# Kernel tuning notes

Hardware: AMD Instinct MI355X
Metric: run time of the kernel (lower is better)

The kernel has to match this reference:

```python
import jax, jax.numpy as jnp
import numpy as np

N_NODES = 100000
N_EDGES = 3200000
N_FEAT = 256
N_CLASS = 4


def setup_inputs() -> dict:
    key = jax.random.key(0)
    ks = jax.random.split(key, 8)
    x = jax.random.normal(ks[0], (N_NODES, N_FEAT), dtype=jnp.float32)
    edge_index = jax.random.randint(ks[1], (2, N_EDGES), 0, N_NODES, dtype=jnp.int64)
    def xavier(k, shape):
        fan_in, fan_out = shape
        std = np.sqrt(2.0 / (fan_in + fan_out))
        return jax.random.normal(k, shape, dtype=jnp.float32) * std
    return {
        'x': x,
        'edge_index': edge_index,
        'W_gcn': xavier(ks[2], (N_FEAT, 64)),
        'b_gcn': jnp.zeros((64,), jnp.float32),
        'W1': xavier(ks[3], (64, 32)),
        'b1': jnp.zeros((32,), jnp.float32),
        'W2': xavier(ks[4], (32, 16)),
        'b2': jnp.zeros((16,), jnp.float32),
        'W3': xavier(ks[5], (16, N_CLASS)),
        'b3': jnp.zeros((N_CLASS,), jnp.float32),
    }


def gcn_conv(x, edge_index, W, b):
    # PyG GCNConv: transform, add self-loops, symmetric normalization, scatter-add
    N = x.shape[0]
    h = x @ W  # [N, 64]
    loop = jnp.arange(N, dtype=edge_index.dtype)
    src = jnp.concatenate([edge_index[0], loop])
    dst = jnp.concatenate([edge_index[1], loop])
    deg = jax.ops.segment_sum(jnp.ones_like(dst, dtype=h.dtype), dst, num_segments=N)
    dinv = jnp.where(deg > 0, jax.lax.rsqrt(deg), 0.0)
    norm = dinv[src] * dinv[dst]  # [E+N]
    msgs = h[src] * norm[:, None]  # gather [E+N, 64]
    out = jax.ops.segment_sum(msgs, dst, num_segments=N)
    return out + b


def reference(x, edge_index, W_gcn, b_gcn, W1, b1, W2, b2, W3, b3):
    h = gcn_conv(x, edge_index, W_gcn, b_gcn)
    h = jax.nn.relu(h)          # dropout is identity in eval mode
    h = jax.nn.relu(h @ W1 + b1)
    h = jax.nn.relu(h @ W2 + b2)
    h = h @ W3 + b3
    return jax.nn.log_softmax(h, axis=1)
```

## Files before the change

### kernel.cpp

```cpp
#include <hip/hip_runtime.h>
#include <hip/hip_bf16.h>

#define NN 100000
#define NE 3200000
#define NPB 64
#define NB 1564
#define CAP 2560
#define BATCH 8192
#define NGB 1563

typedef __hip_bfloat16 bf16;
typedef __attribute__((ext_vector_type(8))) short bf16x8;
typedef __attribute__((ext_vector_type(4))) float f32x4;

__device__ __forceinline__ void fma4(float4& a, float s, const float4 w) {
  a.x = fmaf(s, w.x, a.x);
  a.y = fmaf(s, w.y, a.y);
  a.z = fmaf(s, w.z, a.z);
  a.w = fmaf(s, w.w, a.w);
}

__device__ __forceinline__ unsigned short f2b(float f) {
  unsigned u = __float_as_uint(f);
  unsigned r = ((u >> 16) & 1u) + 0x7FFFu;
  return (unsigned short)((u + r) >> 16);
}

__device__ __forceinline__ unsigned pack2(float lo, float hi) {
  return (unsigned)f2b(lo) | ((unsigned)f2b(hi) << 16);
}

__global__ __launch_bounds__(1024) void bin_k(const void* __restrict__ eidx,
                                              int* __restrict__ bcur,
                                              int* __restrict__ buckets) {
  __shared__ int scnt[NB];
  __shared__ int sofs[NB];
  __shared__ int sbase[NB];
  __shared__ int lcur[NB];
  __shared__ int tot;
  __shared__ int sflag;
  __shared__ int sorted[BATCH];
  __shared__ int gaddr[BATCH];
  int t = threadIdx.x;
  long long e0 = (long long)blockIdx.x * BATCH;
  int m = (int)((NE - e0 < BATCH) ? (NE - e0) : BATCH);

  if (t < 64) {
    unsigned long long bb = __ballot(((const int*)eidx)[2 * t + 1] == 0);
    if (t == 0) sflag = (bb == 0xFFFFFFFFFFFFFFFFULL) ? 1 : 0;
  }
  for (int i = t; i < NB; i += 1024) scnt[i] = 0;
  if (t == 0) tot = 0;
  __syncthreads();
  int isI64 = sflag;

  int ent[BATCH / 1024], bv[BATCH / 1024];
#pragma unroll
  for (int j = 0; j < BATCH / 1024; j++) {
    int idx = t + j * 1024;
    bv[j] = -1;
    if (idx < m) {
      long long i = e0 + idx;
      int s, d;
      if (isI64) {
        s = (int)((const long long*)eidx)[i];
        d = (int)((const long long*)eidx)[NE + i];
      } else {
        s = ((const int*)eidx)[i];
        d = ((const int*)eidx)[NE + i];
      }
      bv[j] = d >> 6;
      ent[j] = s | ((d & 63) << 17);
      atomicAdd(&scnt[bv[j]], 1);
    }
  }
  __syncthreads();
  for (int i = t; i < NB; i += 1024) {
    int c = scnt[i];
    if (c) {
      sofs[i] = atomicAdd(&tot, c);
      sbase[i] = atomicAdd(&bcur[i], c);
      lcur[i] = sofs[i];
    }
  }
  __syncthreads();
#pragma unroll
  for (int j = 0; j < BATCH / 1024; j++) {
    if (bv[j] >= 0) {
      int pos = atomicAdd(&lcur[bv[j]], 1);
      sorted[pos] = ent[j];
      int gp = sbase[bv[j]] + (pos - sofs[bv[j]]);
      gaddr[pos] = (gp < CAP) ? bv[j] * CAP + gp : -1;
    }
  }
  __syncthreads();
  for (int i = t; i < m; i += 1024) {
    int ga = gaddr[i];
    if (ga >= 0) buckets[ga] = sorted[i];
  }
}

__global__ __launch_bounds__(256) void cnt_k(const int* __restrict__ buckets,
                                             const int* __restrict__ bcur,
                                             float* __restrict__ dinv,
                                             const float* __restrict__ W,
                                             unsigned short* __restrict__ wh,
                                             unsigned short* __restrict__ wl) {
  int b = blockIdx.x, t = threadIdx.x;
  if (b == NB) {
#pragma unroll 4
    for (int i = 0; i < 64; i++) {
      int idx = i * 256 + t;
      int j = idx & 7;
      int lane = (idx >> 3) & 63;
      int pair = idx >> 9;
      int nf = pair & 3, kk = pair >> 2;
      int k = kk * 32 + (lane >> 4) * 8 + j;
      int n = nf * 16 + (lane & 15);
      float w = W[k * 64 + n];
      unsigned short hh = f2b(w);
      float fh = __uint_as_float((unsigned)hh << 16);
      wh[idx] = hh;
      wl[idx] = f2b(w - fh);
    }
    return;
  }
  __shared__ int c4[4][NPB];
  int w = t >> 6;
  if (t < 128) { c4[0][t & 63] = 0; c4[1][t & 63] = 0; }
  else         { c4[2][t & 63] = 0; c4[3][t & 63] = 0; }
  __syncthreads();
  int m = bcur[b]; if (m > CAP) m = CAP;
  const int* bp = buckets + (size_t)b * CAP;
  for (int i = t; i < m; i += 256) atomicAdd(&c4[w][(bp[i] >> 17) & 63], 1);
  __syncthreads();
  int node = b * NPB + t;
  if (t < NPB && node < NN) {
    int s = c4[0][t] + c4[1][t] + c4[2][t] + c4[3][t];
    dinv[node] = rsqrtf((float)s + 1.0f);
  }
}

__global__ __launch_bounds__(256) void gemm_k(const float* __restrict__ x,
                                              const unsigned short* __restrict__ wh,
                                              const unsigned short* __restrict__ wl,
                                              const float* __restrict__ dinv,
                                              bf16* __restrict__ h) {
  int t = threadIdx.x;
  int wv = t >> 6, l = t & 63;
  int rowbase = blockIdx.x * 64 + wv * 16;
  int arow = rowbase + (l & 15);
  if (arow >= NN) arow = NN - 1;
  const float* xrow = x + (size_t)arow * 256 + (l >> 4) * 8;

  const bf16x8* whf = (const bf16x8*)wh;
  const bf16x8* wlf = (const bf16x8*)wl;

  f32x4 acc0 = {0.f, 0.f, 0.f, 0.f};
  f32x4 acc1 = acc0, acc2 = acc0, acc3 = acc0;

  float4 x0a = *(const float4*)(xrow +   0), x0b = *(const float4*)(xrow +   4);
  float4 x1a = *(const float4*)(xrow +  32), x1b = *(const float4*)(xrow +  36);
  float4 x2a = *(const float4*)(xrow +  64), x2b = *(const float4*)(xrow +  68);
  float4 x3a = *(const float4*)(xrow +  96), x3b = *(const float4*)(xrow + 100);
  float4 x4a = *(const float4*)(xrow + 128), x4b = *(const float4*)(xrow + 132);
  float4 x5a = *(const float4*)(xrow + 160), x5b = *(const float4*)(xrow + 164);
  float4 x6a = *(const float4*)(xrow + 192), x6b = *(const float4*)(xrow + 196);
  float4 x7a = *(const float4*)(xrow + 224), x7b = *(const float4*)(xrow + 228);

  bf16x8 ha0, ha1, ha2, ha3, la0, la1, la2, la3;
  bf16x8 hb0, hb1, hb2, hb3, lb0, lb1, lb2, lb3;

#define LOADW(H0, H1, H2, H3, L0, L1, L2, L3, kk)                      \
  {                                                                    \
    int fb_ = (kk) * 256 + l;                                          \
    H0 = whf[fb_]; H1 = whf[fb_ + 64]; H2 = whf[fb_ + 128]; H3 = whf[fb_ + 192]; \
    L0 = wlf[fb_]; L1 = wlf[fb_ + 64]; L2 = wlf[fb_ + 128]; L3 = wlf[fb_ + 192]; \
  }
#define COMPUTE(Xa, Xb, H0, H1, H2, H3, L0, L1, L2, L3)                \
  {                                                                    \
    bf16x8 ah, al;                                                     \
    {                                                                  \
      unsigned short hh_; float fh_;                                   \
      hh_ = f2b(Xa.x); fh_ = __uint_as_float((unsigned)hh_ << 16); ah[0] = (short)hh_; al[0] = (short)f2b(Xa.x - fh_); \
      hh_ = f2b(Xa.y); fh_ = __uint_as_float((unsigned)hh_ << 16); ah[1] = (short)hh_; al[1] = (short)f2b(Xa.y - fh_); \
      hh_ = f2b(Xa.z); fh_ = __uint_as_float((unsigned)hh_ << 16); ah[2] = (short)hh_; al[2] = (short)f2b(Xa.z - fh_); \
      hh_ = f2b(Xa.w); fh_ = __uint_as_float((unsigned)hh_ << 16); ah[3] = (short)hh_; al[3] = (short)f2b(Xa.w - fh_); \
      hh_ = f2b(Xb.x); fh_ = __uint_as_float((unsigned)hh_ << 16); ah[4] = (short)hh_; al[4] = (short)f2b(Xb.x - fh_); \
      hh_ = f2b(Xb.y); fh_ = __uint_as_float((unsigned)hh_ << 16); ah[5] = (short)hh_; al[5] = (short)f2b(Xb.y - fh_); \
      hh_ = f2b(Xb.z); fh_ = __uint_as_float((unsigned)hh_ << 16); ah[6] = (short)hh_; al[6] = (short)f2b(Xb.z - fh_); \
      hh_ = f2b(Xb.w); fh_ = __uint_as_float((unsigned)hh_ << 16); ah[7] = (short)hh_; al[7] = (short)f2b(Xb.w - fh_); \
    }                                                                  \
    acc0 = __builtin_amdgcn_mfma_f32_16x16x32_bf16(ah, H0, acc0, 0, 0, 0); \
    acc1 = __builtin_amdgcn_mfma_f32_16x16x32_bf16(ah, H1, acc1, 0, 0, 0); \
    acc2 = __builtin_amdgcn_mfma_f32_16x16x32_bf16(ah, H2, acc2, 0, 0, 0); \
    acc3 = __builtin_amdgcn_mfma_f32_16x16x32_bf16(ah, H3, acc3, 0, 0, 0); \
    acc0 = __builtin_amdgcn_mfma_f32_16x16x32_bf16(ah, L0, acc0, 0, 0, 0); \
    acc1 = __builtin_amdgcn_mfma_f32_16x16x32_bf16(ah, L1, acc1, 0, 0, 0); \
    acc2 = __builtin_amdgcn_mfma_f32_16x16x32_bf16(ah, L2, acc2, 0, 0, 0); \
    acc3 = __builtin_amdgcn_mfma_f32_16x16x32_bf16(ah, L3, acc3, 0, 0, 0); \
    acc0 = __builtin_amdgcn_mfma_f32_16x16x32_bf16(al, H0, acc0, 0, 0, 0); \
    acc1 = __builtin_amdgcn_mfma_f32_16x16x32_bf16(al, H1, acc1, 0, 0, 0); \
    acc2 = __builtin_amdgcn_mfma_f32_16x16x32_bf16(al, H2, acc2, 0, 0, 0); \
    acc3 = __builtin_amdgcn_mfma_f32_16x16x32_bf16(al, H3, acc3, 0, 0, 0); \
  }
#define SBAR __builtin_amdgcn_sched_barrier(0);

  LOADW(ha0, ha1, ha2, ha3, la0, la1, la2, la3, 0)
  LOADW(hb0, hb1, hb2, hb3, lb0, lb1, lb2, lb3, 1)
  COMPUTE(x0a, x0b, ha0, ha1, ha2, ha3, la0, la1, la2, la3) SBAR
  LOADW(ha0, ha1, ha2, ha3, la0, la1, la2, la3, 2)
  COMPUTE(x1a, x1b, hb0, hb1, hb2, hb3, lb0, lb1, lb2, lb3) SBAR
  LOADW(hb0, hb1, hb2, hb3, lb0, lb1, lb2, lb3, 3)
  COMPUTE(x2a, x2b, ha0, ha1, ha2, ha3, la0, la1, la2, la3) SBAR
  LOADW(ha0, ha1, ha2, ha3, la0, la1, la2, la3, 4)
  COMPUTE(x3a, x3b, hb0, hb1, hb2, hb3, lb0, lb1, lb2, lb3) SBAR
  LOADW(hb0, hb1, hb2, hb3, lb0, lb1, lb2, lb3, 5)
  COMPUTE(x4a, x4b, ha0, ha1, ha2, ha3, la0, la1, la2, la3) SBAR
  LOADW(ha0, ha1, ha2, ha3, la0, la1, la2, la3, 6)
  COMPUTE(x5a, x5b, hb0, hb1, hb2, hb3, lb0, lb1, lb2, lb3) SBAR
  LOADW(hb0, hb1, hb2, hb3, lb0, lb1, lb2, lb3, 7)
  COMPUTE(x6a, x6b, ha0, ha1, ha2, ha3, la0, la1, la2, la3) SBAR
  COMPUTE(x7a, x7b, hb0, hb1, hb2, hb3, lb0, lb1, lb2, lb3)
#undef LOADW
#undef COMPUTE
#undef SBAR

#pragma unroll
  for (int reg = 0; reg < 4; reg++) {
    int row = rowbase + (l >> 4) * 4 + reg;
    if (row < NN) {
      float dn = dinv[row];
      unsigned short* hp = (unsigned short*)h + (size_t)row * 64 + (l & 15);
      hp[0]  = f2b(acc0[reg] * dn);
      hp[16] = f2b(acc1[reg] * dn);
      hp[32] = f2b(acc2[reg] * dn);
      hp[48] = f2b(acc3[reg] * dn);
    }
  }
}

__global__ __launch_bounds__(512) void agg_k(const bf16* __restrict__ h,
                                             const int* __restrict__ buckets,
                                             const int* __restrict__ bcur,
                                             const float* __restrict__ dinv,
                                             const float* __restrict__ bg,
                                             bf16* __restrict__ hg) {
  __shared__ int ents[CAP];
  __shared__ int srt[CAP];
  __shared__ int cnt8[8][NPB];
  __shared__ int wcur[8][NPB];
  __shared__ int cnt[NPB];
  __shared__ int off[NPB];
  int b = blockIdx.x, t = threadIdx.x;
  int w = t >> 6;
  int m = bcur[b]; if (m > CAP) m = CAP;
  const int* bp = buckets + (size_t)b * CAP;
  for (int i = t; i < 8 * NPB; i += 512) ((int*)cnt8)[i] = 0;
  __syncthreads();
  for (int i = t; i < m; i += 512) {
    int e = bp[i];
    ents[i] = e;
    atomicAdd(&cnt8[w][(e >> 17) & 63], 1);
  }
  __syncthreads();
  if (t < NPB) {
    int s = 0;
#pragma unroll
    for (int ww = 0; ww < 8; ww++) { int c = cnt8[ww][t]; wcur[ww][t] = s; s += c; }
    cnt[t] = s;
  }
  __syncthreads();
  if (t == 0) {
    int s = 0;
#pragma unroll
    for (int i = 0; i < NPB; i++) { off[i] = s; s += cnt[i]; }
  }
  __syncthreads();
  if (t < NPB) {
#pragma unroll
    for (int ww = 0; ww < 8; ww++) wcur[ww][t] += off[t];
  }
  __syncthreads();
  for (int i = t; i < m; i += 512) {
    int e = ents[i];
    int pos = atomicAdd(&wcur[w][(e >> 17) & 63], 1);
    srt[pos] = e & 0x1FFFF;
  }
  __syncthreads();

  int g = t >> 3, fl = t & 7;
  int node = b * NPB + g;
  if (node >= NN) return;
  int start = off[g];
  int deg = cnt[g];
  float dn = dinv[node];
  const unsigned short* hu = (const unsigned short*)h;

  float a0 = 0.f, a1 = 0.f, a2 = 0.f, a3 = 0.f,
        a4 = 0.f, a5 = 0.f, a6 = 0.f, a7 = 0.f;

#define ACCV(V)                                                          \
  {                                                                      \
    a0 += __uint_as_float(V.x << 16); a1 += __uint_as_float(V.x & 0xFFFF0000u); \
    a2 += __uint_as_float(V.y << 16); a3 += __uint_as_float(V.y & 0xFFFF0000u); \
    a4 += __uint_as_float(V.z << 16); a5 += __uint_as_float(V.z & 0xFFFF0000u); \
    a6 += __uint_as_float(V.w << 16); a7 += __uint_as_float(V.w & 0xFFFF0000u); \
  }

  int i = 0;
  for (; i + 4 <= deg; i += 4) {
    int s0 = srt[start + i], s1 = srt[start + i + 1];
    int s2 = srt[start + i + 2], s3 = srt[start + i + 3];
    uint4 v0 = *(const uint4*)(hu + (size_t)s0 * 64 + fl * 8);
    uint4 v1 = *(const uint4*)(hu + (size_t)s1 * 64 + fl * 8);
    uint4 v2 = *(const uint4*)(hu + (size_t)s2 * 64 + fl * 8);
    uint4 v3 = *(const uint4*)(hu + (size_t)s3 * 64 + fl * 8);
    ACCV(v0) ACCV(v1) ACCV(v2) ACCV(v3)
  }
  for (; i < deg; i++) {
    int s0 = srt[start + i];
    uint4 v0 = *(const uint4*)(hu + (size_t)s0 * 64 + fl * 8);
    ACCV(v0)
  }
#undef ACCV

  uint4 sv = *(const uint4*)(hu + (size_t)node * 64 + fl * 8);
  const float* bb = bg + fl * 8;
  a0 += __uint_as_float(sv.x << 16); a1 += __uint_as_float(sv.x & 0xFFFF0000u);
  a2 += __uint_as_float(sv.y << 16); a3 += __uint_as_float(sv.y & 0xFFFF0000u);
  a4 += __uint_as_float(sv.z << 16); a5 += __uint_as_float(sv.z & 0xFFFF0000u);
  a6 += __uint_as_float(sv.w << 16); a7 += __uint_as_float(sv.w & 0xFFFF0000u);
  uint4 o;
  o.x = pack2(fmaxf(fmaf(a0, dn, bb[0]), 0.f), fmaxf(fmaf(a1, dn, bb[1]), 0.f));
  o.y = pack2(fmaxf(fmaf(a2, dn, bb[2]), 0.f), fmaxf(fmaf(a3, dn, bb[3]), 0.f));
  o.z = pack2(fmaxf(fmaf(a4, dn, bb[4]), 0.f), fmaxf(fmaf(a5, dn, bb[5]), 0.f));
  o.w = pack2(fmaxf(fmaf(a6, dn, bb[6]), 0.f), fmaxf(fmaf(a7, dn, bb[7]), 0.f));
  *(uint4*)((unsigned short*)hg + (size_t)node * 64 + fl * 8) = o;
}

__global__ __launch_bounds__(256) void mlp_k(const bf16* __restrict__ hg,
                                             const float* __restrict__ W1, const float* __restrict__ b1,
                                             const float* __restrict__ W2, const float* __restrict__ b2,
                                             const float* __restrict__ W3, const float* __restrict__ b3,
                                             float* __restrict__ out) {
  __shared__ float4 sW1[512];
  __shared__ float4 sW2[128];
  __shared__ float4 sW3[16];
  __shared__ float sb1[32], sb2[16], sb3[4];
  int t = threadIdx.x;
  for (int i = t; i < 512; i += 256) sW1[i] = ((const float4*)W1)[i];
  if (t < 128) sW2[t] = ((const float4*)W2)[t];
  if (t < 16)  sW3[t] = ((const float4*)W3)[t];
  if (t < 32)  sb1[t] = b1[t];
  if (t < 16)  sb2[t] = b2[t];
  if (t < 4)   sb3[t] = b3[t];
  __syncthreads();
  int n = blockIdx.x * 256 + t;
  if (n >= NN) return;
  float xr[64];
  const uint4* hp = (const uint4*)(hg + (size_t)n * 64);
#pragma unroll
  for (int i = 0; i < 8; i++) {
    uint4 v = hp[i];
    unsigned uu[4] = {v.x, v.y, v.z, v.w};
#pragma unroll
    for (int j = 0; j < 4; j++) {
      xr[8 * i + 2 * j]     = __uint_as_float(uu[j] << 16);
      xr[8 * i + 2 * j + 1] = __uint_as_float(uu[j] & 0xFFFF0000u);
    }
  }
  float4 a1[8];
#pragma unroll
  for (int j = 0; j < 8; j++) a1[j] = make_float4(sb1[4 * j], sb1[4 * j + 1], sb1[4 * j + 2], sb1[4 * j + 3]);
#pragma unroll
  for (int f = 0; f < 64; f++) {
    float xv = xr[f];
#pragma unroll
    for (int j = 0; j < 8; j++) fma4(a1[j], xv, sW1[f * 8 + j]);
  }
  float r2[32];
#pragma unroll
  for (int j = 0; j < 8; j++) {
    r2[4 * j + 0] = fmaxf(a1[j].x, 0.f);
    r2[4 * j + 1] = fmaxf(a1[j].y, 0.f);
    r2[4 * j + 2] = fmaxf(a1[j].z, 0.f);
    r2[4 * j + 3] = fmaxf(a1[j].w, 0.f);
  }
  float4 a2[4];
#pragma unroll
  for (int j = 0; j < 4; j++) a2[j] = make_float4(sb2[4 * j], sb2[4 * j + 1], sb2[4 * j + 2], sb2[4 * j + 3]);
#pragma unroll
  for (int f = 0; f < 32; f++) {
    float xv = r2[f];
#pragma unroll
    for (int j = 0; j < 4; j++) fma4(a2[j], xv, sW2[f * 4 + j]);
  }
  float r3[16];
#pragma unroll
  for (int j = 0; j < 4; j++) {
    r3[4 * j + 0] = fmaxf(a2[j].x, 0.f);
    r3[4 * j + 1] = fmaxf(a2[j].y, 0.f);
    r3[4 * j + 2] = fmaxf(a2[j].z, 0.f);
    r3[4 * j + 3] = fmaxf(a2[j].w, 0.f);
  }
  float4 a3 = make_float4(sb3[0], sb3[1], sb3[2], sb3[3]);
#pragma unroll
  for (int f = 0; f < 16; f++) fma4(a3, r3[f], sW3[f]);
  float m = fmaxf(fmaxf(a3.x, a3.y), fmaxf(a3.z, a3.w));
  float s = expf(a3.x - m) + expf(a3.y - m) + expf(a3.z - m) + expf(a3.w - m);
  float l = m + logf(s);
  ((float4*)out)[n] = make_float4(a3.x - l, a3.y - l, a3.z - l, a3.w - l);
}

extern "C" void kernel_launch(void* const* d_in, const int* in_sizes, int n_in,
                              void* d_out, int out_size, void* d_ws, size_t ws_size,
                              hipStream_t stream) {
  const float* x  = (const float*)d_in[0];
  const void* eidx = d_in[1];
  const float* Wg = (const float*)d_in[2];
  const float* bg = (const float*)d_in[3];
  const float* W1 = (const float*)d_in[4];
  const float* b1 = (const float*)d_in[5];
  const float* W2 = (const float*)d_in[6];
  const float* b2 = (const float*)d_in[7];
  const float* W3 = (const float*)d_in[8];
  const float* b3 = (const float*)d_in[9];

  char* ws = (char*)d_ws;
  bf16*  h       = (bf16*) (ws + 0);
  bf16*  hg      = (bf16*) (ws + 12800000);
  int*   buckets = (int*)  (ws + 25600000);
  float* dinv    = (float*)(ws + 41615360);
  int*   bcur    = (int*)  (ws + 42415360);
  unsigned short* wh = (unsigned short*)(ws + 12800000);
  unsigned short* wl = (unsigned short*)(ws + 12800000 + 32768);

  hipMemsetAsync(bcur, 0, NB * sizeof(int), stream);
  bin_k<<<(NE + BATCH - 1) / BATCH, 1024, 0, stream>>>(eidx, bcur, buckets);
  cnt_k<<<NB + 1, 256, 0, stream>>>(buckets, bcur, dinv, Wg, wh, wl);
  gemm_k<<<NGB, 256, 0, stream>>>(x, wh, wl, dinv, h);
  agg_k<<<NB, 512, 0, stream>>>(h, buckets, bcur, dinv, bg, hg);
  mlp_k<<<(NN + 255) / 256, 256, 0, stream>>>(hg, W1, b1, W2, b2, W3, b3, (float*)d_out);
}
```

Baseline: 152.3 us.

## Fuse MLP head into aggregation kernel and halve edge binning batch

The MLP and log-softmax head now run inside the aggregation kernel. Each block stages its 64 aggregated rows in fp32 shared memory and lets one wavefront run the three small dense layers per node. This removes the bf16 round trip of hg through global memory and one kernel launch. In exchange only 64 of 512 threads do the MLP work, LDS use grows (about 26 KB more), and occupancy may drop. The binning batch size is also halved, giving bin_k more blocks.

```diff
diff --git a/kernel.cpp b/kernel.cpp
--- a/kernel.cpp
+++ b/kernel.cpp
@@ -6,7 +6,7 @@
 #define NPB 64
 #define NB 1564
 #define CAP 2560
-#define BATCH 8192
+#define BATCH 4096
 #define NGB 1563
 
 typedef __hip_bfloat16 bf16;
@@ -245,17 +245,31 @@
                                              const int* __restrict__ bcur,
                                              const float* __restrict__ dinv,
                                              const float* __restrict__ bg,
-                                             bf16* __restrict__ hg) {
+                                             const float* __restrict__ W1, const float* __restrict__ b1,
+                                             const float* __restrict__ W2, const float* __restrict__ b2,
+                                             const float* __restrict__ W3, const float* __restrict__ b3,
+                                             float* __restrict__ out) {
   __shared__ int ents[CAP];
   __shared__ int srt[CAP];
   __shared__ int cnt8[8][NPB];
   __shared__ int wcur[8][NPB];
   __shared__ int cnt[NPB];
   __shared__ int off[NPB];
+  __shared__ float hrowf[NPB][65];
+  __shared__ float4 sW1f[512];
+  __shared__ float4 sW2f[128];
+  __shared__ float4 sW3f[16];
+  __shared__ float sb1[32], sb2[16], sb3[4];
   int b = blockIdx.x, t = threadIdx.x;
   int w = t >> 6;
   int m = bcur[b]; if (m > CAP) m = CAP;
   const int* bp = buckets + (size_t)b * CAP;
+  if (t < 512) sW1f[t] = ((const float4*)W1)[t];
+  if (t < 128) sW2f[t] = ((const float4*)W2)[t];
+  if (t < 16)  sW3f[t] = ((const float4*)W3)[t];
+  if (t < 32)  sb1[t] = b1[t];
+  if (t < 16)  sb2[t] = b2[t];
+  if (t < 4)   sb3[t] = b3[t];
   for (int i = t; i < 8 * NPB; i += 512) ((int*)cnt8)[i] = 0;
   __syncthreads();
   for (int i = t; i < m; i += 512) {
@@ -291,10 +305,9 @@
 
   int g = t >> 3, fl = t & 7;
   int node = b * NPB + g;
-  if (node >= NN) return;
-  int start = off[g];
-  int deg = cnt[g];
-  float dn = dinv[node];
+  bool valid = node < NN;
+  int start = valid ? off[g] : 0;
+  int deg = valid ? cnt[g] : 0;
   const unsigned short* hu = (const unsigned short*)h;
 
   float a0 = 0.f, a1 = 0.f, a2 = 0.f, a3 = 0.f,
@@ -325,92 +338,74 @@
   }
 #undef ACCV
 
-  uint4 sv = *(const uint4*)(hu + (size_t)node * 64 + fl * 8);
-  const float* bb = bg + fl * 8;
-  a0 += __uint_as_float(sv.x << 16); a1 += __uint_as_float(sv.x & 0xFFFF0000u);
-  a2 += __uint_as_float(sv.y << 16); a3 += __uint_as_float(sv.y & 0xFFFF0000u);
-  a4 += __uint_as_float(sv.z << 16); a5 += __uint_as_float(sv.z & 0xFFFF0000u);
-  a6 += __uint_as_float(sv.w << 16); a7 += __uint_as_float(sv.w & 0xFFFF0000u);
-  uint4 o;
-  o.x = pack2(fmaxf(fmaf(a0, dn, bb[0]), 0.f), fmaxf(fmaf(a1, dn, bb[1]), 0.f));
-  o.y = pack2(fmaxf(fmaf(a2, dn, bb[2]), 0.f), fmaxf(fmaf(a3, dn, bb[3]), 0.f));
-  o.z = pack2(fmaxf(fmaf(a4, dn, bb[4]), 0.f), fmaxf(fmaf(a5, dn, bb[5]), 0.f));
-  o.w = pack2(fmaxf(fmaf(a6, dn, bb[6]), 0.f), fmaxf(fmaf(a7, dn, bb[7]), 0.f));
-  *(uint4*)((unsigned short*)hg + (size_t)node * 64 + fl * 8) = o;
-}
-
-__global__ __launch_bounds__(256) void mlp_k(const bf16* __restrict__ hg,
-                                             const float* __restrict__ W1, const float* __restrict__ b1,
-                                             const float* __restrict__ W2, const float* __restrict__ b2,
-                                             const float* __restrict__ W3, const float* __restrict__ b3,
-                                             float* __restrict__ out) {
-  __shared__ float4 sW1[512];
-  __shared__ float4 sW2[128];
-  __shared__ float4 sW3[16];
-  __shared__ float sb1[32], sb2[16], sb3[4];
-  int t = threadIdx.x;
-  for (int i = t; i < 512; i += 256) sW1[i] = ((const float4*)W1)[i];
-  if (t < 128) sW2[t] = ((const float4*)W2)[t];
-  if (t < 16)  sW3[t] = ((const float4*)W3)[t];
-  if (t < 32)  sb1[t] = b1[t];
-  if (t < 16)  sb2[t] = b2[t];
-  if (t < 4)   sb3[t] = b3[t];
-  __syncthreads();
-  int n = blockIdx.x * 256 + t;
-  if (n >= NN) return;
-  float xr[64];
-  const uint4* hp = (const uint4*)(hg + (size_t)n * 64);
-#pragma unroll
-  for (int i = 0; i < 8; i++) {
-    uint4 v = hp[i];
-    unsigned uu[4] = {v.x, v.y, v.z, v.w};
-#pragma unroll
-    for (int j = 0; j < 4; j++) {
-      xr[8 * i + 2 * j]     = __uint_as_float(uu[j] << 16);
-      xr[8 * i + 2 * j + 1] = __uint_as_float(uu[j] & 0xFFFF0000u);
-    }
-  }
-  float4 a1[8];
-#pragma unroll
-  for (int j = 0; j < 8; j++) a1[j] = make_float4(sb1[4 * j], sb1[4 * j + 1], sb1[4 * j + 2], sb1[4 * j + 3]);
-#pragma unroll
-  for (int f = 0; f < 64; f++) {
-    float xv = xr[f];
-#pragma unroll
-    for (int j = 0; j < 8; j++) fma4(a1[j], xv, sW1[f * 8 + j]);
-  }
-  float r2[32];
-#pragma unroll
-  for (int j = 0; j < 8; j++) {
-    r2[4 * j + 0] = fmaxf(a1[j].x, 0.f);
-    r2[4 * j + 1] = fmaxf(a1[j].y, 0.f);
-    r2[4 * j + 2] = fmaxf(a1[j].z, 0.f);
-    r2[4 * j + 3] = fmaxf(a1[j].w, 0.f);
-  }
-  float4 a2[4];
-#pragma unroll
-  for (int j = 0; j < 4; j++) a2[j] = make_float4(sb2[4 * j], sb2[4 * j + 1], sb2[4 * j + 2], sb2[4 * j + 3]);
-#pragma unroll
-  for (int f = 0; f < 32; f++) {
-    float xv = r2[f];
-#pragma unroll
-    for (int j = 0; j < 4; j++) fma4(a2[j], xv, sW2[f * 4 + j]);
-  }
-  float r3[16];
-#pragma unroll
-  for (int j = 0; j < 4; j++) {
-    r3[4 * j + 0] = fmaxf(a2[j].x, 0.f);
-    r3[4 * j + 1] = fmaxf(a2[j].y, 0.f);
-    r3[4 * j + 2] = fmaxf(a2[j].z, 0.f);
-    r3[4 * j + 3] = fmaxf(a2[j].w, 0.f);
-  }
-  float4 a3 = make_float4(sb3[0], sb3[1], sb3[2], sb3[3]);
-#pragma unroll
-  for (int f = 0; f < 16; f++) fma4(a3, r3[f], sW3[f]);
-  float m = fmaxf(fmaxf(a3.x, a3.y), fmaxf(a3.z, a3.w));
-  float s = expf(a3.x - m) + expf(a3.y - m) + expf(a3.z - m) + expf(a3.w - m);
-  float l = m + logf(s);
-  ((float4*)out)[n] = make_float4(a3.x - l, a3.y - l, a3.z - l, a3.w - l);
+  if (valid) {
+    float dn = dinv[node];
+    uint4 sv = *(const uint4*)(hu + (size_t)node * 64 + fl * 8);
+    const float* bb = bg + fl * 8;
+    a0 += __uint_as_float(sv.x << 16); a1 += __uint_as_float(sv.x & 0xFFFF0000u);
+    a2 += __uint_as_float(sv.y << 16); a3 += __uint_as_float(sv.y & 0xFFFF0000u);
+    a4 += __uint_as_float(sv.z << 16); a5 += __uint_as_float(sv.z & 0xFFFF0000u);
+    a6 += __uint_as_float(sv.w << 16); a7 += __uint_as_float(sv.w & 0xFFFF0000u);
+    float* hr = &hrowf[g][fl * 8];
+    hr[0] = fmaxf(fmaf(a0, dn, bb[0]), 0.f);
+    hr[1] = fmaxf(fmaf(a1, dn, bb[1]), 0.f);
+    hr[2] = fmaxf(fmaf(a2, dn, bb[2]), 0.f);
+    hr[3] = fmaxf(fmaf(a3, dn, bb[3]), 0.f);
+    hr[4] = fmaxf(fmaf(a4, dn, bb[4]), 0.f);
+    hr[5] = fmaxf(fmaf(a5, dn, bb[5]), 0.f);
+    hr[6] = fmaxf(fmaf(a6, dn, bb[6]), 0.f);
+    hr[7] = fmaxf(fmaf(a7, dn, bb[7]), 0.f);
+  }
+  __syncthreads();
+
+  if (t < 64) {
+    int nodem = b * NPB + t;
+    if (nodem < NN) {
+      float4 m1[8];
+#pragma unroll
+      for (int j = 0; j < 8; j++)
+        m1[j] = make_float4(sb1[4 * j], sb1[4 * j + 1], sb1[4 * j + 2], sb1[4 * j + 3]);
+#pragma unroll
+      for (int f = 0; f < 64; f++) {
+        float xv = hrowf[t][f];
+#pragma unroll
+        for (int j = 0; j < 8; j++) fma4(m1[j], xv, sW1f[f * 8 + j]);
+      }
+      float r2[32];
+#pragma unroll
+      for (int j = 0; j < 8; j++) {
+        r2[4 * j + 0] = fmaxf(m1[j].x, 0.f);
+        r2[4 * j + 1] = fmaxf(m1[j].y, 0.f);
+        r2[4 * j + 2] = fmaxf(m1[j].z, 0.f);
+        r2[4 * j + 3] = fmaxf(m1[j].w, 0.f);
+      }
+      float4 m2[4];
+#pragma unroll
+      for (int j = 0; j < 4; j++)
+        m2[j] = make_float4(sb2[4 * j], sb2[4 * j + 1], sb2[4 * j + 2], sb2[4 * j + 3]);
+#pragma unroll
+      for (int f = 0; f < 32; f++) {
+        float xv = r2[f];
+#pragma unroll
+        for (int j = 0; j < 4; j++) fma4(m2[j], xv, sW2f[f * 4 + j]);
+      }
+      float r3[16];
+#pragma unroll
+      for (int j = 0; j < 4; j++) {
+        r3[4 * j + 0] = fmaxf(m2[j].x, 0.f);
+        r3[4 * j + 1] = fmaxf(m2[j].y, 0.f);
+        r3[4 * j + 2] = fmaxf(m2[j].z, 0.f);
+        r3[4 * j + 3] = fmaxf(m2[j].w, 0.f);
+      }
+      float4 m3 = make_float4(sb3[0], sb3[1], sb3[2], sb3[3]);
+#pragma unroll
+      for (int f = 0; f < 16; f++) fma4(m3, r3[f], sW3f[f]);
+      float mx = fmaxf(fmaxf(m3.x, m3.y), fmaxf(m3.z, m3.w));
+      float s = expf(m3.x - mx) + expf(m3.y - mx) + expf(m3.z - mx) + expf(m3.w - mx);
+      float lg = mx + logf(s);
+      ((float4*)out)[nodem] = make_float4(m3.x - lg, m3.y - lg, m3.z - lg, m3.w - lg);
+    }
+  }
 }
 
 extern "C" void kernel_launch(void* const* d_in, const int* in_sizes, int n_in,
@@ -429,7 +424,6 @@
 
   char* ws = (char*)d_ws;
   bf16*  h       = (bf16*) (ws + 0);
-  bf16*  hg      = (bf16*) (ws + 12800000);
   int*   buckets = (int*)  (ws + 25600000);
   float* dinv    = (float*)(ws + 41615360);
   int*   bcur    = (int*)  (ws + 42415360);
@@ -440,6 +434,5 @@
   bin_k<<<(NE + BATCH - 1) / BATCH, 1024, 0, stream>>>(eidx, bcur, buckets);
   cnt_k<<<NB + 1, 256, 0, stream>>>(buckets, bcur, dinv, Wg, wh, wl);
   gemm_k<<<NGB, 256, 0, stream>>>(x, wh, wl, dinv, h);
-  agg_k<<<NB, 512, 0, stream>>>(h, buckets, bcur, dinv, bg, hg);
-  mlp_k<<<(NN + 255) / 256, 256, 0, stream>>>(hg, W1, b1, W2, b2, W3, b3, (float*)d_out);
-}
+  agg_k<<<NB, 512, 0, stream>>>(h, buckets, bcur, dinv, bg, W1, b1, W2, b2, W3, b3, (float*)d_out);
+}
```

Result: slower. 177.1 us (+16.3%).
